# Optimization experiments

Hardware: AMD Instinct MI355X
Metric: run time of the kernel (lower is better)

Reference implementation:

```python
import jax, jax.numpy as jnp
import numpy as np


def gcn_conv(x, src, dst, W, b, num_nodes):
    """PyG GCNConv: add self-loops, symmetric deg^-1/2 normalization,
    linear transform, sum-aggregate messages at targets, add bias."""
    loop = jnp.arange(num_nodes, dtype=src.dtype)
    s = jnp.concatenate([src, loop])  # row (source)
    d = jnp.concatenate([dst, loop])  # col (target)
    ones = jnp.ones(d.shape[0], dtype=x.dtype)
    deg = jax.ops.segment_sum(ones, d, num_segments=num_nodes)
    dinv = jnp.where(deg > 0, jax.lax.rsqrt(deg), 0.0)
    norm = dinv[s] * dinv[d]  # [E+N]
    h = x @ W  # [N, hidden]
    msg = h[s] * norm[:, None]  # [E+N, hidden]
    out = jax.ops.segment_sum(msg, d, num_segments=num_nodes)
    return out + b


def setup_inputs() -> dict:
    key = jax.random.key(0)
    ks = jax.random.split(key, 10)
    N, E, G = 50000, 800000, 2048
    IN, H, C = 2, 64, 3
    x = jax.random.normal(ks[0], (N, IN), dtype=jnp.float32)
    edge_index = jax.random.randint(ks[1], (2, E), 0, N, dtype=jnp.int64)
    batch = jnp.sort(jax.random.randint(ks[2], (N,), 0, G, dtype=jnp.int64))
    def glorot(k, shape):
        lim = float(np.sqrt(6.0 / (shape[0] + shape[1])))
        return jax.random.uniform(k, shape, jnp.float32, -lim, lim)
    return {
        "x": x,
        "W1": glorot(ks[3], (IN, H)), "b1": jnp.zeros((H,), jnp.float32),
        "W2": glorot(ks[4], (H, H)), "b2": jnp.zeros((H,), jnp.float32),
        "Wc": glorot(ks[5], (H, C)), "bc": jnp.zeros((C,), jnp.float32),
        "edge_index": edge_index,
        "batch": batch,
        "num_graphs": G,
    }


def reference(x, W1, b1, W2, b2, Wc, bc, edge_index, batch, num_graphs):
    N = x.shape[0]
    # nan_to_num guard, then per-feature standardization (torch std is ddof=1)
    x = jnp.nan_to_num(x, nan=0.0, posinf=0.0, neginf=0.0)
    mu = x.mean(axis=0)
    x = x - mu
    std = jnp.sqrt(jnp.sum(x * x, axis=0) / (N - 1))
    x = x / (std + 1e-6)
    src, dst = edge_index[0], edge_index[1]
    x = jax.nn.relu(gcn_conv(x, src, dst, W1, b1, N))
    x = jax.nn.relu(gcn_conv(x, src, dst, W2, b2, N))
    # global mean pool per graph
    sums = jax.ops.segment_sum(x, batch, num_segments=num_graphs)
    cnt = jax.ops.segment_sum(jnp.ones((N,), x.dtype), batch, num_segments=num_graphs)
    pooled = sums / jnp.maximum(cnt, 1.0)[:, None]  # [G, hidden]
    return pooled @ Wc + bc  # [G, num_classes]
```

## Files before the change

kernel.cpp:

```cpp
#include <hip/hip_runtime.h>
#include <math.h>


#define H 64
#define NB 256
#define NBLK 256

__device__ __forceinline__ float nan0(float v) {
    return isfinite(v) ? v : 0.0f;
}

__device__ __forceinline__ int ld_idx(const void* p, long long i, int is64) {
    if (is64) return (int)((const long long*)p)[i];
    return ((const int*)p)[i];
}

__global__ __launch_bounds__(256) void k_pre(
    const float* __restrict__ x, int N, float4* __restrict__ stats_part,
    const void* ei, int E, const int* batch, int nB, int* flags,
    unsigned* __restrict__ packed, int* __restrict__ histM) {
    if (blockIdx.x < 128) {
        if (blockIdx.x == 0) {
            __shared__ int nz_b;
            if (threadIdx.x == 0) nz_b = 0;
            __syncthreads();
            long long pb = 1 + 2 * ((long long)threadIdx.x * ((nB - 2) / 2) / 256);
            if (pb < nB && batch[pb] != 0) nz_b = 1;
            __syncthreads();
            if (threadIdx.x == 0) flags[1] = (nz_b == 0);
        }
        float s0 = 0, s1 = 0, q0 = 0, q1 = 0;
        int tid = blockIdx.x * blockDim.x + threadIdx.x;
        int stride = 128 * blockDim.x;
        for (int n = tid; n < N; n += stride) {
            float2 v = reinterpret_cast<const float2*>(x)[n];
            float a = nan0(v.x), b = nan0(v.y);
            s0 += a; s1 += b; q0 += a * a; q1 += b * b;
        }
        for (int m = 32; m >= 1; m >>= 1) {
            s0 += __shfl_down(s0, m);
            s1 += __shfl_down(s1, m);
            q0 += __shfl_down(q0, m);
            q1 += __shfl_down(q1, m);
        }
        __shared__ float red[4][4];
        int w = threadIdx.x >> 6, lane = threadIdx.x & 63;
        if (lane == 0) { red[w][0] = s0; red[w][1] = s1; red[w][2] = q0; red[w][3] = q1; }
        __syncthreads();
        if (threadIdx.x == 0) {
            float t0 = 0, t1 = 0, t2 = 0, t3 = 0;
            for (int i = 0; i < 4; i++) {
                t0 += red[i][0]; t1 += red[i][1]; t2 += red[i][2]; t3 += red[i][3];
            }
            stats_part[blockIdx.x] = make_float4(t0, t1, t2, t3);
        }
    } else {
        int blk = blockIdx.x - 128;
        int beg = (int)((long long)blk * E / NBLK);
        int end = (int)((long long)(blk + 1) * E / NBLK);
        __shared__ int hist[NB];
        __shared__ int nz_e;
        if (threadIdx.x == 0) nz_e = 0;
        for (int i = threadIdx.x; i < NB; i += 256) hist[i] = 0;
        __syncthreads();
        if (threadIdx.x < 64) {
            int span = end - beg;
            long long p = 2LL * beg + 1 +
                          2 * ((long long)threadIdx.x * (span > 1 ? span - 1 : 0) / 64);
            if (((const int*)ei)[p] != 0) nz_e = 1;
        }
        __syncthreads();
        int is64 = (nz_e == 0);
        for (int e = beg + threadIdx.x; e < end; e += 256) {
            unsigned s = (unsigned)ld_idx(ei, e, is64);
            unsigned d = (unsigned)ld_idx(ei, (long long)E + e, is64);
            packed[e] = (d << 16) | s;
            atomicAdd(&hist[d >> 8], 1);
        }
        __syncthreads();
        for (int i = threadIdx.x; i < NB; i += 256)
            histM[i * NBLK + blk] = hist[i];
    }
}

__global__ __launch_bounds__(256) void k_scanA(int* __restrict__ histM,
                                               int* __restrict__ bsum,
                                               const float4* __restrict__ stats_part,
                                               float* __restrict__ stats) {
    __shared__ int tmp[NBLK];
    int f = blockIdx.x * NBLK + threadIdx.x;
    int v = histM[f];
    tmp[threadIdx.x] = v;
    if (blockIdx.x == 0) {
        __shared__ float4 sred[128];
        if (threadIdx.x < 128) sred[threadIdx.x] = stats_part[threadIdx.x];
        __syncthreads();
        for (int off = 64; off >= 1; off >>= 1) {
            if (threadIdx.x < off) {
                sred[threadIdx.x].x += sred[threadIdx.x + off].x;
                sred[threadIdx.x].y += sred[threadIdx.x + off].y;
                sred[threadIdx.x].z += sred[threadIdx.x + off].z;
                sred[threadIdx.x].w += sred[threadIdx.x + off].w;
            }
            __syncthreads();
        }
        if (threadIdx.x == 0) *reinterpret_cast<float4*>(stats) = sred[0];
    } else {
        __syncthreads();
    }
    __syncthreads();
    for (int off = 1; off < NBLK; off <<= 1) {
        int t = (threadIdx.x >= off) ? tmp[threadIdx.x - off] : 0;
        __syncthreads();
        tmp[threadIdx.x] += t;
        __syncthreads();
    }
    histM[f] = tmp[threadIdx.x] - v;
    if (threadIdx.x == NBLK - 1) bsum[blockIdx.x] = tmp[NBLK - 1];
}

__global__ __launch_bounds__(256) void k_part(const unsigned* __restrict__ packed,
                                              const int* __restrict__ histM,
                                              const int* __restrict__ bsum,
                                              unsigned* __restrict__ binned,
                                              int E) {
    __shared__ int sb[NB];
    __shared__ int cur[NB];
    int blk = blockIdx.x;
    int v = bsum[threadIdx.x];
    sb[threadIdx.x] = v;
    __syncthreads();
    for (int off = 1; off < NB; off <<= 1) {
        int t = (threadIdx.x >= off) ? sb[threadIdx.x - off] : 0;
        __syncthreads();
        sb[threadIdx.x] += t;
        __syncthreads();
    }
    cur[threadIdx.x] = (sb[threadIdx.x] - v) + histM[threadIdx.x * NBLK + blk];
    __syncthreads();
    int beg = (int)((long long)blk * E / NBLK);
    int end = (int)((long long)(blk + 1) * E / NBLK);
    for (int e = beg + threadIdx.x; e < end; e += 256) {
        unsigned p = packed[e];
        int pos = atomicAdd(&cur[p >> 24], 1);
        binned[pos] = p;
    }
}

__global__ __launch_bounds__(256) void k_bsort(
    const unsigned* __restrict__ binned, const int* __restrict__ bsum,
    unsigned short* __restrict__ csr16, int* __restrict__ counts,
    int* __restrict__ offsets, const float* __restrict__ x,
    const float* __restrict__ stats, float2* __restrict__ T, int N, int E) {
    __shared__ int hist[NB], tmp[NB], cur[NB];
    __shared__ int sbeg, send;
    int b = blockIdx.x;
    {
        int v = bsum[threadIdx.x];
        tmp[threadIdx.x] = v;
        __syncthreads();
        for (int off = 1; off < NB; off <<= 1) {
            int t = (threadIdx.x >= off) ? tmp[threadIdx.x - off] : 0;
            __syncthreads();
            tmp[threadIdx.x] += t;
            __syncthreads();
        }
        if (threadIdx.x == b) { sbeg = tmp[threadIdx.x] - v; send = tmp[threadIdx.x]; }
    }
    __syncthreads();
    int beg = sbeg, end = send;
    hist[threadIdx.x] = 0;
    __syncthreads();
    for (int i = beg + threadIdx.x; i < end; i += 256)
        atomicAdd(&hist[(binned[i] >> 16) & 0xff], 1);
    __syncthreads();
    int v = hist[threadIdx.x];
    tmp[threadIdx.x] = v;
    __syncthreads();
    for (int off = 1; off < NB; off <<= 1) {
        int t = (threadIdx.x >= off) ? tmp[threadIdx.x - off] : 0;
        __syncthreads();
        tmp[threadIdx.x] += t;
        __syncthreads();
    }
    int ex = tmp[threadIdx.x] - v;
    cur[threadIdx.x] = ex;
    int n = b * NB + threadIdx.x;
    if (n < N) {
        counts[n] = v;
        offsets[n] = beg + ex;
        float sum0 = stats[0], sum1 = stats[1], q0 = stats[2], q1 = stats[3];
        float mu0 = sum0 / N, mu1 = sum1 / N;
        float v0 = fmaxf((q0 - sum0 * sum0 / N) / (N - 1), 0.0f);
        float v1 = fmaxf((q1 - sum1 * sum1 / N) / (N - 1), 0.0f);
        float r0 = 1.0f / (sqrtf(v0) + 1e-6f);
        float r1 = 1.0f / (sqrtf(v1) + 1e-6f);
        float di = rsqrtf((float)(v + 1));
        float2 xv = reinterpret_cast<const float2*>(x)[n];
        T[n] = make_float2(di * (nan0(xv.x) - mu0) * r0,
                           di * (nan0(xv.y) - mu1) * r1);
    }
    if (n == N) offsets[N] = E;
    __syncthreads();
    for (int i = beg + threadIdx.x; i < end; i += 256) {
        unsigned p = binned[i];
        int t = atomicAdd(&cur[(p >> 16) & 0xff], 1);
        csr16[beg + t] = (unsigned short)(p & 0xffffu);
    }
}

__global__ void k_aggQ(const unsigned short* __restrict__ csr16,
                       const int* __restrict__ offsets,
                       const float2* __restrict__ T,
                       const int* __restrict__ counts,
                       float4* __restrict__ Q, int N) {
    int t = blockIdx.x * blockDim.x + threadIdx.x;
    int n = t >> 3, sub = t & 7;
    if (n >= N) return;
    int beg = offsets[n], end = offsets[n + 1];
    float s0 = 0.0f, s1 = 0.0f;
    for (int k = beg + sub; k < end; k += 8) {
        float2 ts = T[csr16[k]];
        s0 += ts.x; s1 += ts.y;
    }
    s0 += __shfl_xor(s0, 1); s1 += __shfl_xor(s1, 1);
    s0 += __shfl_xor(s0, 2); s1 += __shfl_xor(s1, 2);
    s0 += __shfl_xor(s0, 4); s1 += __shfl_xor(s1, 4);
    if (sub == 0) {
        float di = rsqrtf((float)(counts[n] + 1));
        float2 tn = T[n];
        s0 += tn.x; s1 += tn.y;
        Q[n] = make_float4(s0 * di * di, s1 * di * di, di, 0.0f);
    }
}

__global__ __launch_bounds__(512, 6) void k_gathgemm(
    const unsigned short* __restrict__ csr16, const int* __restrict__ offsets,
    const float4* __restrict__ Q, const float* __restrict__ W1,
    const float* __restrict__ b1, const float* __restrict__ W2,
    const float* __restrict__ b2, float* __restrict__ Bout, int N) {
    __shared__ float At[64][68];
    __shared__ float Ws[64][64];
    __shared__ float bs[64];
    __shared__ float4 chunkW[8][2][64];
    __shared__ float4 qrow[8][8];
    __shared__ int    rend[8][8];
    int tid = threadIdx.x;
    for (int i = tid; i < 64 * 64; i += 512) Ws[i >> 6][i & 63] = W2[i];
    if (tid < 64) bs[tid] = b2[tid];
    int rbase = blockIdx.x * 64;
    int wid = tid >> 6, j = tid & 63;
    float w10 = W1[j], w11 = W1[H + j], bb = b1[j];

    int r0 = min(rbase + wid * 8, N);
    int r1 = min(r0 + 8, N);
    if (r0 < r1) {
        if (j < 8 && r0 + j < r1) {
            qrow[wid][j] = Q[r0 + j];
            rend[wid][j] = offsets[r0 + j + 1];
        }
        int eBeg = offsets[r0], eEnd = offsets[r1];
        int row = 0;
        float4 qd = qrow[wid][0];
        int rowEnd = rend[wid][0];
        float di = qd.z;
        float acc = fmaxf(qd.x * w10 + qd.y * w11 + qd.z * bb, 0.0f);
        if (eBeg + j < eEnd) chunkW[wid][0][j] = Q[csr16[eBeg + j]];
        int buf = 0;
        for (int base = eBeg; base < eEnd; base += 64) {
            int nbase = base + 64;
            bool hasNext = nbase < eEnd;
            float4 qn;
            if (hasNext && nbase + j < eEnd) qn = Q[csr16[nbase + j]];
            int cnt = min(64, eEnd - base);
            int k = 0;
            for (; k + 4 <= cnt; k += 4) {
                float4 q0 = chunkW[wid][buf][k + 0];
                float4 q1 = chunkW[wid][buf][k + 1];
                float4 q2 = chunkW[wid][buf][k + 2];
                float4 q3 = chunkW[wid][buf][k + 3];
                float t0 = fmaxf(q0.x * w10 + q0.y * w11 + q0.z * bb, 0.0f);
                float t1 = fmaxf(q1.x * w10 + q1.y * w11 + q1.z * bb, 0.0f);
                float t2 = fmaxf(q2.x * w10 + q2.y * w11 + q2.z * bb, 0.0f);
                float t3 = fmaxf(q3.x * w10 + q3.y * w11 + q3.z * bb, 0.0f);
                int e0 = base + k;
#pragma unroll
                for (int i = 0; i < 4; i++) {
                    while (e0 + i >= rowEnd) {
                        At[j][(r0 - rbase) + row] = di * acc;
                        row++;
                        rowEnd = rend[wid][row];
                        qd = qrow[wid][row];
                        di = qd.z;
                        acc = fmaxf(qd.x * w10 + qd.y * w11 + qd.z * bb, 0.0f);
                    }
                    acc += (i == 0) ? t0 : (i == 1) ? t1 : (i == 2) ? t2 : t3;
                }
            }
            for (; k < cnt; k++) {
                float4 q = chunkW[wid][buf][k];
                float tt = fmaxf(q.x * w10 + q.y * w11 + q.z * bb, 0.0f);
                int ecur = base + k;
                while (ecur >= rowEnd) {
                    At[j][(r0 - rbase) + row] = di * acc;
                    row++;
                    rowEnd = rend[wid][row];
                    qd = qrow[wid][row];
                    di = qd.z;
                    acc = fmaxf(qd.x * w10 + qd.y * w11 + qd.z * bb, 0.0f);
                }
                acc += tt;
            }
            if (hasNext) {
                if (nbase + j < eEnd) chunkW[wid][buf ^ 1][j] = qn;
                buf ^= 1;
            }
        }
        while (true) {
            At[j][(r0 - rbase) + row] = di * acc;
            row++;
            if (r0 + row >= r1) break;
            qd = qrow[wid][row];
            di = qd.z;
            acc = fmaxf(qd.x * w10 + qd.y * w11 + qd.z * bb, 0.0f);
        }
    }
    __syncthreads();
    int kh = tid >> 8;
    int idx = tid & 255;
    int rg = (idx >> 4) * 4;
    int cg = (idx & 15) * 4;
    float a4[4][4] = {{0.0f}};
#pragma unroll 8
    for (int k = kh * 32; k < kh * 32 + 32; k++) {
        float4 a = *reinterpret_cast<const float4*>(&At[k][rg]);
        float4 b = *reinterpret_cast<const float4*>(&Ws[k][cg]);
        a4[0][0] += a.x * b.x; a4[0][1] += a.x * b.y;
        a4[0][2] += a.x * b.z; a4[0][3] += a.x * b.w;
        a4[1][0] += a.y * b.x; a4[1][1] += a.y * b.y;
        a4[1][2] += a.y * b.z; a4[1][3] += a.y * b.w;
        a4[2][0] += a.z * b.x; a4[2][1] += a.z * b.y;
        a4[2][2] += a.z * b.z; a4[2][3] += a.z * b.w;
        a4[3][0] += a.w * b.x; a4[3][1] += a.w * b.y;
        a4[3][2] += a.w * b.z; a4[3][3] += a.w * b.w;
    }
    __syncthreads();
    float* comb = reinterpret_cast<float*>(chunkW);
    if (kh == 1) {
#pragma unroll
        for (int i = 0; i < 16; i++)
            comb[i * 256 + idx] = a4[i >> 2][i & 3];
    }
    __syncthreads();
    if (kh == 0) {
#pragma unroll
        for (int i = 0; i < 16; i++)
            a4[i >> 2][i & 3] += comb[i * 256 + idx];
#pragma unroll
        for (int i2 = 0; i2 < 4; i2++) {
            int r = rbase + rg + i2;
            if (r < N) {
                *reinterpret_cast<float4*>(&Bout[(size_t)r * H + cg]) =
                    make_float4(fmaxf(a4[i2][0] + bs[cg + 0], 0.0f),
                                fmaxf(a4[i2][1] + bs[cg + 1], 0.0f),
                                fmaxf(a4[i2][2] + bs[cg + 2], 0.0f),
                                fmaxf(a4[i2][3] + bs[cg + 3], 0.0f));
            }
        }
    }
}

__global__ __launch_bounds__(256) void k_poolcls(
    const float* __restrict__ B, const void* batch,
    const float* __restrict__ Wc, const float* __restrict__ bc,
    float* __restrict__ out, int N, int G, const int* __restrict__ flags) {
    int t = blockIdx.x * blockDim.x + threadIdx.x;
    int g = t >> 6, j = t & 63;
    if (g >= G) return;
    int is64 = flags[1];
    int beg, end;
    {
        int lo = 0, hi = N;
        while (lo < hi) {
            int mid = (lo + hi) >> 1;
            if (ld_idx(batch, mid, is64) < g) lo = mid + 1; else hi = mid;
        }
        beg = lo;
    }
    {
        int lo = beg, hi = N;
        while (lo < hi) {
            int mid = (lo + hi) >> 1;
            if (ld_idx(batch, mid, is64) < g + 1) lo = mid + 1; else hi = mid;
        }
        end = lo;
    }
    float a0 = 0, a1 = 0, a2 = 0, a3 = 0;
    int n = beg;
    for (; n + 4 <= end; n += 4) {
        a0 += B[(size_t)(n + 0) * H + j];
        a1 += B[(size_t)(n + 1) * H + j];
        a2 += B[(size_t)(n + 2) * H + j];
        a3 += B[(size_t)(n + 3) * H + j];
    }
    for (; n < end; n++) a0 += B[(size_t)n * H + j];
    float acc = (a0 + a1) + (a2 + a3);
    float p = acc / (float)max(end - beg, 1);
#pragma unroll
    for (int c = 0; c < 3; c++) {
        float v = p * Wc[j * 3 + c];
        for (int m = 32; m >= 1; m >>= 1) v += __shfl_xor(v, m);
        if (j == 0) out[g * 3 + c] = v + bc[c];
    }
}

extern "C" void kernel_launch(void* const* d_in, const int* in_sizes, int n_in,
                              void* d_out, int out_size, void* d_ws,
                              size_t ws_size, hipStream_t stream) {
    const float* x  = (const float*)d_in[0];
    const float* W1 = (const float*)d_in[1];
    const float* b1 = (const float*)d_in[2];
    const float* W2 = (const float*)d_in[3];
    const float* b2 = (const float*)d_in[4];
    const float* Wc = (const float*)d_in[5];
    const float* bc = (const float*)d_in[6];
    const void*  ei = d_in[7];
    const void*  batch = d_in[8];

    int N = in_sizes[0] / 2;
    int E = in_sizes[7] / 2;
    int G = out_size / 3;

    float4* Q       = (float4*)d_ws;
    float4* stats_part = Q + N;
    float*  B       = (float*)(stats_part + 128);
    float2* T       = (float2*)(B + (size_t)N * H);
    unsigned* packed = (unsigned*)(T + N);
    unsigned* binned = packed + E;
    unsigned short* csr16 = (unsigned short*)(binned + E);
    int*    histM   = (int*)(csr16 + ((E + 1) & ~1));
    int*    counts  = histM + NB * NBLK;
    int*    offsets = counts + N;
    int*    bsum    = offsets + N + 1;
    float*  stats   = (float*)(bsum + NB);
    int*    flags   = (int*)(stats + 8);

    float* out = (float*)d_out;

    k_pre<<<384, 256, 0, stream>>>(x, N, stats_part, ei, E,
                                   (const int*)batch, in_sizes[8], flags,
                                   packed, histM);
    k_scanA<<<NB, NBLK, 0, stream>>>(histM, bsum, stats_part, stats);
    k_part<<<NBLK, 256, 0, stream>>>(packed, histM, bsum, binned, E);
    k_bsort<<<NB, NB, 0, stream>>>(binned, bsum, csr16, counts, offsets,
                                   x, stats, T, N, E);
    k_aggQ<<<(N * 8 + 255) / 256, 256, 0, stream>>>(csr16, offsets, T, counts,
                                                    Q, N);
    k_gathgemm<<<(N + 63) / 64, 512, 0, stream>>>(csr16, offsets, Q, W1, b1,
                                                  W2, b2, B, N);
    k_poolcls<<<(G * H + 255) / 256, 256, 0, stream>>>(B, batch, Wc, bc, out,
                                                       N, G, flags);
}
```

Before: 91.86 us.

## Fuse CSR build stages into one cooperative kernel with grid syncs

Replaces the four preprocessing kernels (stats and histogram, scan, partition, bucket sort) with a single cooperative kernel of 256 blocks that uses grid.sync between phases. The stats reduction now uses all 256 blocks instead of 128, and each block does both stats and edge packing. This removes three kernel launch boundaries and their gaps, at the cost of grid-wide barrier overhead and the cooperative launch path.

```diff
diff --git a/kernel.cpp b/kernel.cpp
--- a/kernel.cpp
+++ b/kernel.cpp
@@ -1,5 +1,8 @@
 #include <hip/hip_runtime.h>
+#include <hip/hip_cooperative_groups.h>
 #include <math.h>
+
+namespace cg = cooperative_groups;
 
 
 #define H 64
@@ -15,24 +18,35 @@
     return ((const int*)p)[i];
 }
 
-__global__ __launch_bounds__(256) void k_pre(
-    const float* __restrict__ x, int N, float4* __restrict__ stats_part,
-    const void* ei, int E, const int* batch, int nB, int* flags,
-    unsigned* __restrict__ packed, int* __restrict__ histM) {
-    if (blockIdx.x < 128) {
-        if (blockIdx.x == 0) {
+__global__ __launch_bounds__(256) void k_build(
+    const float* __restrict__ x, int N, const void* ei, int E,
+    const int* batch, int nB, int* __restrict__ flags,
+    unsigned* __restrict__ packed, int* __restrict__ histM,
+    int* __restrict__ bsum, float4* __restrict__ stats_part,
+    float* __restrict__ stats, unsigned* __restrict__ binned,
+    unsigned short* __restrict__ csr16, int* __restrict__ counts,
+    int* __restrict__ offsets, float2* __restrict__ T) {
+    cg::grid_group grid = cg::this_grid();
+    int blk = blockIdx.x;
+    int tid = threadIdx.x;
+    __shared__ int sh_a[NB], sh_b[NB], sh_c[NB];
+
+    int eBeg = (int)((long long)blk * E / NBLK);
+    int eEnd = (int)((long long)(blk + 1) * E / NBLK);
+
+    {
+        if (blk == 0) {
             __shared__ int nz_b;
-            if (threadIdx.x == 0) nz_b = 0;
-            __syncthreads();
-            long long pb = 1 + 2 * ((long long)threadIdx.x * ((nB - 2) / 2) / 256);
+            if (tid == 0) nz_b = 0;
+            __syncthreads();
+            long long pb = 1 + 2 * ((long long)tid * ((nB - 2) / 2) / 256);
             if (pb < nB && batch[pb] != 0) nz_b = 1;
             __syncthreads();
-            if (threadIdx.x == 0) flags[1] = (nz_b == 0);
+            if (tid == 0) flags[1] = (nz_b == 0);
         }
         float s0 = 0, s1 = 0, q0 = 0, q1 = 0;
-        int tid = blockIdx.x * blockDim.x + threadIdx.x;
-        int stride = 128 * blockDim.x;
-        for (int n = tid; n < N; n += stride) {
+        int gtid = blk * 256 + tid;
+        for (int n = gtid; n < N; n += 256 * 256) {
             float2 v = reinterpret_cast<const float2*>(x)[n];
             float a = nan0(v.x), b = nan0(v.y);
             s0 += a; s1 += b; q0 += a * a; q1 += b * b;
@@ -44,168 +58,141 @@
             q1 += __shfl_down(q1, m);
         }
         __shared__ float red[4][4];
-        int w = threadIdx.x >> 6, lane = threadIdx.x & 63;
+        int w = tid >> 6, lane = tid & 63;
         if (lane == 0) { red[w][0] = s0; red[w][1] = s1; red[w][2] = q0; red[w][3] = q1; }
-        __syncthreads();
-        if (threadIdx.x == 0) {
+        __shared__ int nz_e;
+        if (tid == 0) nz_e = 0;
+        sh_a[tid] = 0;
+        __syncthreads();
+        if (tid == 0) {
             float t0 = 0, t1 = 0, t2 = 0, t3 = 0;
             for (int i = 0; i < 4; i++) {
                 t0 += red[i][0]; t1 += red[i][1]; t2 += red[i][2]; t3 += red[i][3];
             }
-            stats_part[blockIdx.x] = make_float4(t0, t1, t2, t3);
-        }
-    } else {
-        int blk = blockIdx.x - 128;
-        int beg = (int)((long long)blk * E / NBLK);
-        int end = (int)((long long)(blk + 1) * E / NBLK);
-        __shared__ int hist[NB];
-        __shared__ int nz_e;
-        if (threadIdx.x == 0) nz_e = 0;
-        for (int i = threadIdx.x; i < NB; i += 256) hist[i] = 0;
-        __syncthreads();
-        if (threadIdx.x < 64) {
-            int span = end - beg;
-            long long p = 2LL * beg + 1 +
-                          2 * ((long long)threadIdx.x * (span > 1 ? span - 1 : 0) / 64);
+            stats_part[blk] = make_float4(t0, t1, t2, t3);
+        }
+        if (tid < 64) {
+            int span = eEnd - eBeg;
+            long long p = 2LL * eBeg + 1 +
+                          2 * ((long long)tid * (span > 1 ? span - 1 : 0) / 64);
             if (((const int*)ei)[p] != 0) nz_e = 1;
         }
         __syncthreads();
         int is64 = (nz_e == 0);
-        for (int e = beg + threadIdx.x; e < end; e += 256) {
+        for (int e = eBeg + tid; e < eEnd; e += 256) {
             unsigned s = (unsigned)ld_idx(ei, e, is64);
             unsigned d = (unsigned)ld_idx(ei, (long long)E + e, is64);
             packed[e] = (d << 16) | s;
-            atomicAdd(&hist[d >> 8], 1);
-        }
-        __syncthreads();
-        for (int i = threadIdx.x; i < NB; i += 256)
-            histM[i * NBLK + blk] = hist[i];
-    }
-}
-
-__global__ __launch_bounds__(256) void k_scanA(int* __restrict__ histM,
-                                               int* __restrict__ bsum,
-                                               const float4* __restrict__ stats_part,
-                                               float* __restrict__ stats) {
-    __shared__ int tmp[NBLK];
-    int f = blockIdx.x * NBLK + threadIdx.x;
-    int v = histM[f];
-    tmp[threadIdx.x] = v;
-    if (blockIdx.x == 0) {
-        __shared__ float4 sred[128];
-        if (threadIdx.x < 128) sred[threadIdx.x] = stats_part[threadIdx.x];
-        __syncthreads();
-        for (int off = 64; off >= 1; off >>= 1) {
-            if (threadIdx.x < off) {
-                sred[threadIdx.x].x += sred[threadIdx.x + off].x;
-                sred[threadIdx.x].y += sred[threadIdx.x + off].y;
-                sred[threadIdx.x].z += sred[threadIdx.x + off].z;
-                sred[threadIdx.x].w += sred[threadIdx.x + off].w;
-            }
-            __syncthreads();
-        }
-        if (threadIdx.x == 0) *reinterpret_cast<float4*>(stats) = sred[0];
-    } else {
-        __syncthreads();
-    }
-    __syncthreads();
-    for (int off = 1; off < NBLK; off <<= 1) {
-        int t = (threadIdx.x >= off) ? tmp[threadIdx.x - off] : 0;
-        __syncthreads();
-        tmp[threadIdx.x] += t;
-        __syncthreads();
-    }
-    histM[f] = tmp[threadIdx.x] - v;
-    if (threadIdx.x == NBLK - 1) bsum[blockIdx.x] = tmp[NBLK - 1];
-}
-
-__global__ __launch_bounds__(256) void k_part(const unsigned* __restrict__ packed,
-                                              const int* __restrict__ histM,
-                                              const int* __restrict__ bsum,
-                                              unsigned* __restrict__ binned,
-                                              int E) {
-    __shared__ int sb[NB];
-    __shared__ int cur[NB];
-    int blk = blockIdx.x;
-    int v = bsum[threadIdx.x];
-    sb[threadIdx.x] = v;
-    __syncthreads();
-    for (int off = 1; off < NB; off <<= 1) {
-        int t = (threadIdx.x >= off) ? sb[threadIdx.x - off] : 0;
-        __syncthreads();
-        sb[threadIdx.x] += t;
-        __syncthreads();
-    }
-    cur[threadIdx.x] = (sb[threadIdx.x] - v) + histM[threadIdx.x * NBLK + blk];
-    __syncthreads();
-    int beg = (int)((long long)blk * E / NBLK);
-    int end = (int)((long long)(blk + 1) * E / NBLK);
-    for (int e = beg + threadIdx.x; e < end; e += 256) {
-        unsigned p = packed[e];
-        int pos = atomicAdd(&cur[p >> 24], 1);
-        binned[pos] = p;
-    }
-}
-
-__global__ __launch_bounds__(256) void k_bsort(
-    const unsigned* __restrict__ binned, const int* __restrict__ bsum,
-    unsigned short* __restrict__ csr16, int* __restrict__ counts,
-    int* __restrict__ offsets, const float* __restrict__ x,
-    const float* __restrict__ stats, float2* __restrict__ T, int N, int E) {
-    __shared__ int hist[NB], tmp[NB], cur[NB];
-    __shared__ int sbeg, send;
-    int b = blockIdx.x;
-    {
-        int v = bsum[threadIdx.x];
-        tmp[threadIdx.x] = v;
+            atomicAdd(&sh_a[d >> 8], 1);
+        }
+        __syncthreads();
+        histM[tid * NBLK + blk] = sh_a[tid];
+    }
+    grid.sync();
+
+    {
+        int f = blk * NBLK + tid;
+        int v = histM[f];
+        sh_a[tid] = v;
+        __syncthreads();
+        for (int off = 1; off < NBLK; off <<= 1) {
+            int t = (tid >= off) ? sh_a[tid - off] : 0;
+            __syncthreads();
+            sh_a[tid] += t;
+            __syncthreads();
+        }
+        histM[f] = sh_a[tid] - v;
+        if (tid == NBLK - 1) bsum[blk] = sh_a[NBLK - 1];
+        if (blk == 0) {
+            __shared__ float4 sred[256];
+            sred[tid] = stats_part[tid];
+            __syncthreads();
+            for (int off = 128; off >= 1; off >>= 1) {
+                if (tid < off) {
+                    sred[tid].x += sred[tid + off].x;
+                    sred[tid].y += sred[tid + off].y;
+                    sred[tid].z += sred[tid + off].z;
+                    sred[tid].w += sred[tid + off].w;
+                }
+                __syncthreads();
+            }
+            if (tid == 0) *reinterpret_cast<float4*>(stats) = sred[0];
+        }
+    }
+    grid.sync();
+
+    {
+        int v = bsum[tid];
+        sh_a[tid] = v;
         __syncthreads();
         for (int off = 1; off < NB; off <<= 1) {
-            int t = (threadIdx.x >= off) ? tmp[threadIdx.x - off] : 0;
-            __syncthreads();
-            tmp[threadIdx.x] += t;
-            __syncthreads();
-        }
-        if (threadIdx.x == b) { sbeg = tmp[threadIdx.x] - v; send = tmp[threadIdx.x]; }
-    }
-    __syncthreads();
-    int beg = sbeg, end = send;
-    hist[threadIdx.x] = 0;
-    __syncthreads();
-    for (int i = beg + threadIdx.x; i < end; i += 256)
-        atomicAdd(&hist[(binned[i] >> 16) & 0xff], 1);
-    __syncthreads();
-    int v = hist[threadIdx.x];
-    tmp[threadIdx.x] = v;
-    __syncthreads();
-    for (int off = 1; off < NB; off <<= 1) {
-        int t = (threadIdx.x >= off) ? tmp[threadIdx.x - off] : 0;
-        __syncthreads();
-        tmp[threadIdx.x] += t;
-        __syncthreads();
-    }
-    int ex = tmp[threadIdx.x] - v;
-    cur[threadIdx.x] = ex;
-    int n = b * NB + threadIdx.x;
-    if (n < N) {
-        counts[n] = v;
-        offsets[n] = beg + ex;
-        float sum0 = stats[0], sum1 = stats[1], q0 = stats[2], q1 = stats[3];
-        float mu0 = sum0 / N, mu1 = sum1 / N;
-        float v0 = fmaxf((q0 - sum0 * sum0 / N) / (N - 1), 0.0f);
-        float v1 = fmaxf((q1 - sum1 * sum1 / N) / (N - 1), 0.0f);
-        float r0 = 1.0f / (sqrtf(v0) + 1e-6f);
-        float r1 = 1.0f / (sqrtf(v1) + 1e-6f);
-        float di = rsqrtf((float)(v + 1));
-        float2 xv = reinterpret_cast<const float2*>(x)[n];
-        T[n] = make_float2(di * (nan0(xv.x) - mu0) * r0,
-                           di * (nan0(xv.y) - mu1) * r1);
-    }
-    if (n == N) offsets[N] = E;
-    __syncthreads();
-    for (int i = beg + threadIdx.x; i < end; i += 256) {
-        unsigned p = binned[i];
-        int t = atomicAdd(&cur[(p >> 16) & 0xff], 1);
-        csr16[beg + t] = (unsigned short)(p & 0xffffu);
+            int t = (tid >= off) ? sh_a[tid - off] : 0;
+            __syncthreads();
+            sh_a[tid] += t;
+            __syncthreads();
+        }
+        sh_b[tid] = (sh_a[tid] - v) + histM[tid * NBLK + blk];
+        __syncthreads();
+        for (int e = eBeg + tid; e < eEnd; e += 256) {
+            unsigned p = packed[e];
+            int pos = atomicAdd(&sh_b[p >> 24], 1);
+            binned[pos] = p;
+        }
+    }
+    grid.sync();
+
+    {
+        int v = bsum[tid];
+        sh_a[tid] = v;
+        __syncthreads();
+        for (int off = 1; off < NB; off <<= 1) {
+            int t = (tid >= off) ? sh_a[tid - off] : 0;
+            __syncthreads();
+            sh_a[tid] += t;
+            __syncthreads();
+        }
+        __shared__ int sbeg, send;
+        if (tid == blk) { sbeg = sh_a[tid] - v; send = sh_a[tid]; }
+        __syncthreads();
+        int beg = sbeg, end = send;
+        sh_b[tid] = 0;
+        __syncthreads();
+        for (int i = beg + tid; i < end; i += 256)
+            atomicAdd(&sh_b[(binned[i] >> 16) & 0xff], 1);
+        __syncthreads();
+        int hv = sh_b[tid];
+        sh_c[tid] = hv;
+        __syncthreads();
+        for (int off = 1; off < NB; off <<= 1) {
+            int t = (tid >= off) ? sh_c[tid - off] : 0;
+            __syncthreads();
+            sh_c[tid] += t;
+            __syncthreads();
+        }
+        int ex = sh_c[tid] - hv;
+        sh_a[tid] = ex;
+        int n = blk * NB + tid;
+        if (n < N) {
+            counts[n] = hv;
+            offsets[n] = beg + ex;
+            float sum0 = stats[0], sum1 = stats[1], q0 = stats[2], q1 = stats[3];
+            float mu0 = sum0 / N, mu1 = sum1 / N;
+            float v0 = fmaxf((q0 - sum0 * sum0 / N) / (N - 1), 0.0f);
+            float v1 = fmaxf((q1 - sum1 * sum1 / N) / (N - 1), 0.0f);
+            float r0 = 1.0f / (sqrtf(v0) + 1e-6f);
+            float r1 = 1.0f / (sqrtf(v1) + 1e-6f);
+            float di = rsqrtf((float)(hv + 1));
+            float2 xv = reinterpret_cast<const float2*>(x)[n];
+            T[n] = make_float2(di * (nan0(xv.x) - mu0) * r0,
+                               di * (nan0(xv.y) - mu1) * r1);
+        }
+        if (n == N) offsets[N] = E;
+        __syncthreads();
+        for (int i = beg + tid; i < end; i += 256) {
+            unsigned p = binned[i];
+            int t = atomicAdd(&sh_a[(p >> 16) & 0xff], 1);
+            csr16[beg + t] = (unsigned short)(p & 0xffffu);
+        }
     }
 }
 
@@ -430,10 +417,11 @@
     int N = in_sizes[0] / 2;
     int E = in_sizes[7] / 2;
     int G = out_size / 3;
+    int nBatch = in_sizes[8];
 
     float4* Q       = (float4*)d_ws;
     float4* stats_part = Q + N;
-    float*  B       = (float*)(stats_part + 128);
+    float*  B       = (float*)(stats_part + 256);
     float2* T       = (float2*)(B + (size_t)N * H);
     unsigned* packed = (unsigned*)(T + N);
     unsigned* binned = packed + E;
@@ -447,13 +435,16 @@
 
     float* out = (float*)d_out;
 
-    k_pre<<<384, 256, 0, stream>>>(x, N, stats_part, ei, E,
-                                   (const int*)batch, in_sizes[8], flags,
-                                   packed, histM);
-    k_scanA<<<NB, NBLK, 0, stream>>>(histM, bsum, stats_part, stats);
-    k_part<<<NBLK, 256, 0, stream>>>(packed, histM, bsum, binned, E);
-    k_bsort<<<NB, NB, 0, stream>>>(binned, bsum, csr16, counts, offsets,
-                                   x, stats, T, N, E);
+    {
+        void* args[] = {(void*)&x, (void*)&N, (void*)&ei, (void*)&E,
+                        (void*)&batch, (void*)&nBatch, (void*)&flags,
+                        (void*)&packed, (void*)&histM, (void*)&bsum,
+                        (void*)&stats_part, (void*)&stats, (void*)&binned,
+                        (void*)&csr16, (void*)&counts, (void*)&offsets,
+                        (void*)&T};
+        hipLaunchCooperativeKernel((void*)k_build, dim3(NBLK), dim3(256),
+                                   args, 0, stream);
+    }
     k_aggQ<<<(N * 8 + 255) / 256, 256, 0, stream>>>(csr16, offsets, T, counts,
                                                     Q, N);
     k_gathgemm<<<(N + 63) / 64, 512, 0, stream>>>(csr16, offsets, Q, W1, b1,
```

After: 203.7 us. 122% more time.
